# Kernel tuning notes

Hardware: AMD Instinct MI355X
Metric: run time of the kernel (lower is better)

Reference implementation:

```python
import jax, jax.numpy as jnp
from jax import lax
import numpy as np

EMBED_DIM = 512
KERNEL_SIZE = 8
B, S = 16, 4096


def setup_inputs() -> dict:
    key = jax.random.key(0)
    k1, k2, k3, k4, k5 = jax.random.split(key, 5)
    bound = 1.0 / np.sqrt(EMBED_DIM)
    x = jax.random.normal(k1, (B, S, EMBED_DIM), dtype=jnp.float32)
    W_ih = jax.random.uniform(k2, (EMBED_DIM, EMBED_DIM), jnp.float32, -bound, bound)
    W_hh = jax.random.uniform(k3, (EMBED_DIM, EMBED_DIM), jnp.float32, -bound, bound)
    b_ih = jax.random.uniform(k4, (EMBED_DIM,), jnp.float32, -bound, bound)
    b_hh = jax.random.uniform(k5, (EMBED_DIM,), jnp.float32, -bound, bound)
    return {"x": x, "W_ih": W_ih, "W_hh": W_hh, "b_ih": b_ih, "b_hh": b_hh}


def reference(x, W_ih, W_hh, b_ih, b_hh):
    # RNNPool.forward(x, mask=False): split seq into windows of KERNEL_SIZE,
    # run a vanilla tanh RNN (zero initial state) on each window, keep last h.
    Bd, Sd, E = x.shape
    stride = KERNEL_SIZE
    nw = Sd // stride
    # All windows are independent -> batch them: [B*nw, stride, E]
    xw = x.reshape(Bd * nw, stride, E)
    # Precompute input projection + both biases once: [B*nw, stride, E]
    pre = jnp.einsum("nte,he->nth", xw, W_ih) + (b_ih + b_hh)

    def step(h, p_t):
        h = jnp.tanh(p_t + h @ W_hh.T)
        return h, None

    h0 = jnp.zeros((Bd * nw, E), dtype=x.dtype)
    hT, _ = lax.scan(step, h0, jnp.swapaxes(pre, 0, 1))  # scan over stride steps
    return hT.reshape(Bd, nw, E)
```

## Files before the change

### kernel.cpp

```cpp
#include <hip/hip_runtime.h>
#include <hip/hip_bf16.h>
#include <stdint.h>


#define E_DIM 512
#define KSIZE 8
#define R_WIN 32
#define R_PRE 64
#define NBLK  256

typedef __attribute__((ext_vector_type(8))) _Float16       f16x8;
typedef __attribute__((ext_vector_type(4))) float          f32x4;
typedef __attribute__((ext_vector_type(4))) float          fv4;
typedef __attribute__((ext_vector_type(4))) unsigned short u16x4;
typedef __attribute__((ext_vector_type(8))) unsigned short u16x8;

typedef __attribute__((address_space(1))) const uint32_t glb_u32;
typedef __attribute__((address_space(3))) uint32_t       lds_u32;

__device__ __forceinline__ unsigned short f2h(float f) {
  return __builtin_bit_cast(unsigned short, (_Float16)f);
}
__device__ __forceinline__ float h2f(unsigned short u) {
  return (float)__builtin_bit_cast(_Float16, u);
}
__device__ __forceinline__ float tanh_fast(float v) {
  return 1.0f - 2.0f / (1.0f + __expf(2.0f * v));
}
__device__ __forceinline__ int swz(int row) { return (row ^ (row >> 1)) & 7; }

__global__ void pack_kernel(const float* __restrict__ Wih, const float* __restrict__ Whh,
                            const float* __restrict__ bih, const float* __restrict__ bhh,
                            unsigned short* __restrict__ wpack, float* __restrict__ bias) {
  int tid = blockIdx.x * 256 + threadIdx.x;
  int l = tid & 63;
  int s = (tid >> 6) & 15;
  int n = (tid >> 10) & 31;
  int m = tid >> 15;
  const float* W = m ? Whh : Wih;
  int row = n * 16 + (l & 15);
  int k0  = s * 32 + (l >> 4) * 8;
  const float* src = W + row * E_DIM + k0;
  u16x8 u;
  #pragma unroll
  for (int j = 0; j < 8; ++j) u[j] = f2h(src[j]);
  size_t dst = (((size_t)m * 16 + s) * 32 + n) * 512 + (size_t)l * 8;
  *reinterpret_cast<u16x8*>(wpack + dst) = u;
  if (tid < E_DIM) bias[tid] = bih[tid] + bhh[tid];
}

#define PRE_FRAG(bt, mt, nt) ((((size_t)(bt) * 2 + (mt)) * 32 + (nt)) * 256)

__global__ __launch_bounds__(512, 2)
void pre_kernel(const float* __restrict__ x,
                const unsigned short* __restrict__ wpack,
                const float* __restrict__ bias,
                unsigned short* __restrict__ prep) {
  __shared__ unsigned short x_lds[R_PRE * E_DIM];

  const int bt   = blockIdx.x;
  const int b    = bt >> 3;
  const int t    = bt & 7;
  const int w0   = b * R_PRE;
  const int tid  = threadIdx.x;
  const int lane = tid & 63;
  const int wid  = tid >> 6;
  const int l15  = lane & 15;
  const int a5   = lane >> 4;
  const int nt0  = wid * 4;

  float bias_r[4];
  #pragma unroll
  for (int n = 0; n < 4; ++n) bias_r[n] = bias[(nt0 + n) * 16 + l15];

  {
    const int srow = tid >> 3;
    const int sc   = tid & 7;
    const fv4* src4 = reinterpret_cast<const fv4*>(
        x + (size_t)((w0 + srow) * KSIZE + t) * E_DIM);
    #pragma unroll
    for (int j = 0; j < 16; ++j) {
      fv4 v = __builtin_nontemporal_load(&src4[sc + 8 * j]);
      int col  = (sc + 8 * j) * 4;
      int idx  = srow * E_DIM + (((col >> 3) ^ swz(srow)) << 3) + (col & 7);
      u16x4 u;
      u[0] = f2h(v.x); u[1] = f2h(v.y); u[2] = f2h(v.z); u[3] = f2h(v.w);
      *reinterpret_cast<u16x4*>(&x_lds[idx]) = u;
    }
  }
  __syncthreads();

  f32x4 acc[4][4];
  #pragma unroll
  for (int m = 0; m < 4; ++m)
    #pragma unroll
    for (int n = 0; n < 4; ++n) acc[m][n] = (f32x4){0.f, 0.f, 0.f, 0.f};

  #pragma unroll
  for (int s = 0; s < 16; ++s) {
    int u0 = s * 4 + a5;
    f16x8 A0, A1, A2, A3;
    {
      int r0 = l15,      i0 = r0 * E_DIM + ((u0 ^ swz(r0)) << 3);
      int r1 = 16 + l15, i1 = r1 * E_DIM + ((u0 ^ swz(r1)) << 3);
      int r2 = 32 + l15, i2 = r2 * E_DIM + ((u0 ^ swz(r2)) << 3);
      int r3 = 48 + l15, i3 = r3 * E_DIM + ((u0 ^ swz(r3)) << 3);
      A0 = *reinterpret_cast<const f16x8*>(&x_lds[i0]);
      A1 = *reinterpret_cast<const f16x8*>(&x_lds[i1]);
      A2 = *reinterpret_cast<const f16x8*>(&x_lds[i2]);
      A3 = *reinterpret_cast<const f16x8*>(&x_lds[i3]);
    }
    const unsigned short* wsl = wpack + ((size_t)s * 32 + nt0) * 512 + lane * 8;
    #pragma unroll
    for (int n = 0; n < 4; ++n) {
      f16x8 Bf = *reinterpret_cast<const f16x8*>(wsl + n * 512);
      acc[0][n] = __builtin_amdgcn_mfma_f32_16x16x32_f16(A0, Bf, acc[0][n], 0, 0, 0);
      acc[1][n] = __builtin_amdgcn_mfma_f32_16x16x32_f16(A1, Bf, acc[1][n], 0, 0, 0);
      acc[2][n] = __builtin_amdgcn_mfma_f32_16x16x32_f16(A2, Bf, acc[2][n], 0, 0, 0);
      acc[3][n] = __builtin_amdgcn_mfma_f32_16x16x32_f16(A3, Bf, acc[3][n], 0, 0, 0);
    }
  }

  #pragma unroll
  for (int m = 0; m < 4; ++m) {
    size_t bt_out = (size_t)(2 * b + (m >> 1)) * 8 + t;
    #pragma unroll
    for (int n = 0; n < 4; ++n) {
      u16x4 v;
      #pragma unroll
      for (int r = 0; r < 4; ++r) v[r] = f2h(acc[m][n][r] + bias_r[n]);
      __builtin_nontemporal_store(v,
          reinterpret_cast<u16x4*>(&prep[PRE_FRAG(bt_out, m & 1, nt0 + n) + lane * 4]));
    }
  }
}

__global__ __launch_bounds__(512, 2)
void rec_kernel(const unsigned short* __restrict__ prep,
                const unsigned short* __restrict__ wpack,
                float* __restrict__ out) {
  __shared__ unsigned short h_buf[2][R_WIN * E_DIM];
  __shared__ unsigned short w_ring[2][8 * 2048];

  const int b    = blockIdx.x;
  const int w0   = b * R_WIN;
  const int tid  = threadIdx.x;
  const int lane = tid & 63;
  const int wid  = tid >> 6;
  const int l15  = lane & 15;
  const int a5   = lane >> 4;
  const int nt0  = wid * 4;

  const char* wbase = (const char*)(wpack + ((size_t)16 * 32) * 512);
  #define STAGE(s, p)                                                               \
    do {                                                                            \
      const char* _src = wbase + (((size_t)(s) * 32 + nt0) * 1024) + lane * 16;     \
      unsigned short* _dst = &w_ring[p][wid * 2048];                                \
      __builtin_amdgcn_global_load_lds((glb_u32*)_src, (lds_u32*)_dst, 16, 0, 0);   \
      __builtin_amdgcn_global_load_lds((glb_u32*)(_src + 1024),                     \
                                       (lds_u32*)(_dst + 512), 16, 0, 0);           \
      __builtin_amdgcn_global_load_lds((glb_u32*)(_src + 2048),                     \
                                       (lds_u32*)(_dst + 1024), 16, 0, 0);          \
      __builtin_amdgcn_global_load_lds((glb_u32*)(_src + 3072),                     \
                                       (lds_u32*)(_dst + 1536), 16, 0, 0);          \
    } while (0)

  #pragma unroll
  for (int mt = 0; mt < 2; ++mt)
    #pragma unroll
    for (int n = 0; n < 4; ++n) {
      u16x4 p = __builtin_nontemporal_load(reinterpret_cast<const u16x4*>(
          &prep[PRE_FRAG(b * 8 + 0, mt, nt0 + n) + lane * 4]));
      int ncol = (nt0 + n) * 16 + l15;
      int ub = ncol >> 3, co = ncol & 7;
      #pragma unroll
      for (int r = 0; r < 4; ++r) {
        int row = mt * 16 + a5 * 4 + r;
        int idx = row * E_DIM + ((ub ^ swz(row)) << 3) + co;
        h_buf[0][idx] = f2h(tanh_fast(h2f(p[r])));
      }
    }

  u16x4 nxt[2][4];
  #pragma unroll
  for (int mt = 0; mt < 2; ++mt)
    #pragma unroll
    for (int n = 0; n < 4; ++n)
      nxt[mt][n] = __builtin_nontemporal_load(reinterpret_cast<const u16x4*>(
          &prep[PRE_FRAG(b * 8 + 1, mt, nt0 + n) + lane * 4]));

  __syncthreads();

  int cur = 0;
  for (int t = 1; t < KSIZE; ++t) {
    f32x4 acc[2][4];
    #pragma unroll
    for (int mt = 0; mt < 2; ++mt)
      #pragma unroll
      for (int n = 0; n < 4; ++n) {
        #pragma unroll
        for (int r = 0; r < 4; ++r) acc[mt][n][r] = h2f(nxt[mt][n][r]);
      }

    STAGE(0, 0);
    STAGE(1, 1);
    asm volatile("s_waitcnt vmcnt(4)" ::: "memory");
    f16x8 Wa0, Wa1, Wa2, Wa3, Ha0, Ha1;
    f16x8 Wb0, Wb1, Wb2, Wb3, Hb0, Hb1;
    {
      const unsigned short* wsl = &w_ring[0][wid * 2048 + lane * 8];
      Wa0 = *reinterpret_cast<const f16x8*>(wsl);
      Wa1 = *reinterpret_cast<const f16x8*>(wsl + 512);
      Wa2 = *reinterpret_cast<const f16x8*>(wsl + 1024);
      Wa3 = *reinterpret_cast<const f16x8*>(wsl + 1536);
      int ia0 = l15 * E_DIM + ((a5 ^ swz(l15)) << 3);
      int ia1 = (16 + l15) * E_DIM + ((a5 ^ swz(16 + l15)) << 3);
      Ha0 = *reinterpret_cast<const f16x8*>(&h_buf[cur][ia0]);
      Ha1 = *reinterpret_cast<const f16x8*>(&h_buf[cur][ia1]);
    }

    #pragma unroll
    for (int s = 0; s < 16; ++s) {
      asm volatile("s_waitcnt lgkmcnt(0)" ::: "memory");
      if (s + 2 < 16) STAGE(s + 2, (s + 2) & 1);
      if (s < 14)       asm volatile("s_waitcnt vmcnt(4)" ::: "memory");
      else if (s == 14) asm volatile("s_waitcnt vmcnt(0)" ::: "memory");
      if (s < 15) {
        const unsigned short* wsl = &w_ring[(s + 1) & 1][wid * 2048 + lane * 8];
        Wb0 = *reinterpret_cast<const f16x8*>(wsl);
        Wb1 = *reinterpret_cast<const f16x8*>(wsl + 512);
        Wb2 = *reinterpret_cast<const f16x8*>(wsl + 1024);
        Wb3 = *reinterpret_cast<const f16x8*>(wsl + 1536);
        int u0  = (s + 1) * 4 + a5;
        int ia0 = l15 * E_DIM + ((u0 ^ swz(l15)) << 3);
        int ia1 = (16 + l15) * E_DIM + ((u0 ^ swz(16 + l15)) << 3);
        Hb0 = *reinterpret_cast<const f16x8*>(&h_buf[cur][ia0]);
        Hb1 = *reinterpret_cast<const f16x8*>(&h_buf[cur][ia1]);
      }
      acc[0][0] = __builtin_amdgcn_mfma_f32_16x16x32_f16(Ha0, Wa0, acc[0][0], 0, 0, 0);
      acc[1][0] = __builtin_amdgcn_mfma_f32_16x16x32_f16(Ha1, Wa0, acc[1][0], 0, 0, 0);
      acc[0][1] = __builtin_amdgcn_mfma_f32_16x16x32_f16(Ha0, Wa1, acc[0][1], 0, 0, 0);
      acc[1][1] = __builtin_amdgcn_mfma_f32_16x16x32_f16(Ha1, Wa1, acc[1][1], 0, 0, 0);
      acc[0][2] = __builtin_amdgcn_mfma_f32_16x16x32_f16(Ha0, Wa2, acc[0][2], 0, 0, 0);
      acc[1][2] = __builtin_amdgcn_mfma_f32_16x16x32_f16(Ha1, Wa2, acc[1][2], 0, 0, 0);
      acc[0][3] = __builtin_amdgcn_mfma_f32_16x16x32_f16(Ha0, Wa3, acc[0][3], 0, 0, 0);
      acc[1][3] = __builtin_amdgcn_mfma_f32_16x16x32_f16(Ha1, Wa3, acc[1][3], 0, 0, 0);
      Wa0 = Wb0; Wa1 = Wb1; Wa2 = Wb2; Wa3 = Wb3;
      Ha0 = Hb0; Ha1 = Hb1;
    }

    if (t == KSIZE - 1) {
      #pragma unroll
      for (int mt = 0; mt < 2; ++mt)
        #pragma unroll
        for (int n = 0; n < 4; ++n) {
          int ncol = (nt0 + n) * 16 + l15;
          #pragma unroll
          for (int r = 0; r < 4; ++r) {
            int row = mt * 16 + a5 * 4 + r;
            out[(size_t)(w0 + row) * E_DIM + ncol] = tanh_fast(acc[mt][n][r]);
          }
        }
    } else {
      #pragma unroll
      for (int mt = 0; mt < 2; ++mt)
        #pragma unroll
        for (int n = 0; n < 4; ++n)
          nxt[mt][n] = __builtin_nontemporal_load(reinterpret_cast<const u16x4*>(
              &prep[PRE_FRAG(b * 8 + t + 1, mt, nt0 + n) + lane * 4]));

      int nb = cur ^ 1;
      #pragma unroll
      for (int mt = 0; mt < 2; ++mt)
        #pragma unroll
        for (int n = 0; n < 4; ++n) {
          int ncol = (nt0 + n) * 16 + l15;
          int ub = ncol >> 3, co = ncol & 7;
          #pragma unroll
          for (int r = 0; r < 4; ++r) {
            int row = mt * 16 + a5 * 4 + r;
            int idx = row * E_DIM + ((ub ^ swz(row)) << 3) + co;
            h_buf[nb][idx] = f2h(tanh_fast(acc[mt][n][r]));
          }
        }
      __syncthreads();
      cur = nb;
    }
  }
  #undef STAGE
}

__global__ __launch_bounds__(512, 1)
void rnnpool_fused(const float* __restrict__ x,
                   const unsigned short* __restrict__ wpack,
                   const float* __restrict__ bias,
                   float* __restrict__ out) {
  __shared__ unsigned short x_lds[R_WIN * E_DIM];
  __shared__ unsigned short h_lds[R_WIN * E_DIM];

  const int tid  = threadIdx.x;
  const int lane = tid & 63;
  const int wid  = tid >> 6;
  const int w0   = blockIdx.x * R_WIN;
  const int l15 = lane & 15;
  const int a5  = lane >> 4;
  const int nt0 = wid * 4;

  float bias_r[4];
  #pragma unroll
  for (int n = 0; n < 4; ++n) bias_r[n] = bias[(nt0 + n) * 16 + l15];

  const int srow = tid >> 4;
  const int sc4  = tid & 15;

  for (int t = 0; t < KSIZE; ++t) {
    {
      const fv4* src4 = reinterpret_cast<const fv4*>(
          x + (size_t)((w0 + srow) * KSIZE + t) * E_DIM);
      #pragma unroll
      for (int j = 0; j < 8; ++j) {
        fv4 v = src4[sc4 + 16 * j];
        int col  = (sc4 + 16 * j) * 4;
        int idx  = srow * E_DIM + (((col >> 3) ^ swz(srow)) << 3) + (col & 7);
        u16x4 u;
        u[0] = f2h(v.x); u[1] = f2h(v.y); u[2] = f2h(v.z); u[3] = f2h(v.w);
        *reinterpret_cast<u16x4*>(&x_lds[idx]) = u;
      }
    }
    __syncthreads();

    f32x4 acc[2][4];
    #pragma unroll
    for (int mt = 0; mt < 2; ++mt)
      #pragma unroll
      for (int n = 0; n < 4; ++n) acc[mt][n] = (f32x4){0.f, 0.f, 0.f, 0.f};

    #pragma unroll
    for (int s = 0; s < 16; ++s) {
      int u0 = s * 4 + a5;
      int ia = l15 * E_DIM + ((u0 ^ swz(l15)) << 3);
      f16x8 A0 = *reinterpret_cast<const f16x8*>(&x_lds[ia]);
      f16x8 A1 = *reinterpret_cast<const f16x8*>(&x_lds[ia + 16 * E_DIM]);
      const unsigned short* wsl = wpack + ((size_t)s * 32 + nt0) * 512 + lane * 8;
      #pragma unroll
      for (int n = 0; n < 4; ++n) {
        f16x8 Bf = *reinterpret_cast<const f16x8*>(wsl + n * 512);
        acc[0][n] = __builtin_amdgcn_mfma_f32_16x16x32_f16(A0, Bf, acc[0][n], 0, 0, 0);
        acc[1][n] = __builtin_amdgcn_mfma_f32_16x16x32_f16(A1, Bf, acc[1][n], 0, 0, 0);
      }
    }

    if (t > 0) {
      #pragma unroll
      for (int s = 0; s < 16; ++s) {
        int u0 = s * 4 + a5;
        int ia = l15 * E_DIM + ((u0 ^ swz(l15)) << 3);
        f16x8 H0 = *reinterpret_cast<const f16x8*>(&h_lds[ia]);
        f16x8 H1 = *reinterpret_cast<const f16x8*>(&h_lds[ia + 16 * E_DIM]);
        const unsigned short* wsl = wpack + ((size_t)(16 + s) * 32 + nt0) * 512 + lane * 8;
        #pragma unroll
        for (int n = 0; n < 4; ++n) {
          f16x8 Bf = *reinterpret_cast<const f16x8*>(wsl + n * 512);
          acc[0][n] = __builtin_amdgcn_mfma_f32_16x16x32_f16(H0, Bf, acc[0][n], 0, 0, 0);
          acc[1][n] = __builtin_amdgcn_mfma_f32_16x16x32_f16(H1, Bf, acc[1][n], 0, 0, 0);
        }
      }
    }
    __syncthreads();

    if (t == KSIZE - 1) {
      #pragma unroll
      for (int mt = 0; mt < 2; ++mt)
        #pragma unroll
        for (int n = 0; n < 4; ++n) {
          int ncol = (nt0 + n) * 16 + l15;
          #pragma unroll
          for (int r = 0; r < 4; ++r) {
            int row = mt * 16 + a5 * 4 + r;
            out[(size_t)(w0 + row) * E_DIM + ncol] = tanh_fast(acc[mt][n][r] + bias_r[n]);
          }
        }
    } else {
      #pragma unroll
      for (int mt = 0; mt < 2; ++mt)
        #pragma unroll
        for (int n = 0; n < 4; ++n) {
          int ncol = (nt0 + n) * 16 + l15;
          int ub = ncol >> 3, co = ncol & 7;
          #pragma unroll
          for (int r = 0; r < 4; ++r) {
            int row = mt * 16 + a5 * 4 + r;
            int idx = row * E_DIM + ((ub ^ swz(row)) << 3) + co;
            h_lds[idx] = f2h(tanh_fast(acc[mt][n][r] + bias_r[n]));
          }
        }
      __syncthreads();
    }
  }
}

extern "C" void kernel_launch(void* const* d_in, const int* in_sizes, int n_in,
                              void* d_out, int out_size, void* d_ws, size_t ws_size,
                              hipStream_t stream) {
  const float* x   = (const float*)d_in[0];
  const float* Wih = (const float*)d_in[1];
  const float* Whh = (const float*)d_in[2];
  const float* bih = (const float*)d_in[3];
  const float* bhh = (const float*)d_in[4];
  float* out = (float*)d_out;

  const size_t PRE_BYTES  = (size_t)33554432 * 2;
  const size_t WPK_BYTES  = (size_t)524288 * 2;
  const size_t NEED       = PRE_BYTES + WPK_BYTES + 4096;

  if (ws_size >= NEED) {
    unsigned short* prep  = (unsigned short*)d_ws;
    unsigned short* wpack = (unsigned short*)((char*)d_ws + PRE_BYTES);
    float*          bias  = (float*)((char*)d_ws + PRE_BYTES + WPK_BYTES);
    pack_kernel<<<256, 256, 0, stream>>>(Wih, Whh, bih, bhh, wpack, bias);
    pre_kernel<<<1024, 512, 0, stream>>>(x, wpack, bias, prep);
    rec_kernel<<<NBLK, 512, 0, stream>>>(prep, wpack, out);
  } else {
    unsigned short* wpack = (unsigned short*)d_ws;
    float*          bias  = (float*)((char*)d_ws + WPK_BYTES);
    pack_kernel<<<256, 256, 0, stream>>>(Wih, Whh, bih, bhh, wpack, bias);
    rnnpool_fused<<<NBLK, 512, 0, stream>>>(x, wpack, bias, out);
  }
}
```

Baseline: 152.8 us.

## Split recurrence blocks to 16 windows each and single-buffer hidden state

The recurrence kernel now handles 16 windows per block instead of 32, launching 512 blocks, and each wave does 4 MFMAs per k-step instead of 8. The hidden-state buffer in LDS drops from double to single buffering, with an extra barrier before it is overwritten, and launch bounds rise to allow 4 blocks per CU. The aim is more parallelism and occupancy across the 256 CUs. In exchange, every weight tile is streamed from L2 twice as often per window, and the extra barrier adds a sync per step.

```diff
diff --git a/kernel.cpp b/kernel.cpp
--- a/kernel.cpp
+++ b/kernel.cpp
@@ -5,9 +5,8 @@
 
 #define E_DIM 512
 #define KSIZE 8
-#define R_WIN 32
+#define R_REC 16
 #define R_PRE 64
-#define NBLK  256
 
 typedef __attribute__((ext_vector_type(8))) _Float16       f16x8;
 typedef __attribute__((ext_vector_type(4))) float          f32x4;
@@ -135,15 +134,17 @@
   }
 }
 
-__global__ __launch_bounds__(512, 2)
+__global__ __launch_bounds__(512, 4)
 void rec_kernel(const unsigned short* __restrict__ prep,
                 const unsigned short* __restrict__ wpack,
                 float* __restrict__ out) {
-  __shared__ unsigned short h_buf[2][R_WIN * E_DIM];
+  __shared__ unsigned short h_buf[R_REC * E_DIM];
   __shared__ unsigned short w_ring[2][8 * 2048];
 
-  const int b    = blockIdx.x;
-  const int w0   = b * R_WIN;
+  const int rb   = blockIdx.x;
+  const int gb   = rb >> 1;
+  const int mtb  = rb & 1;
+  const int w0   = rb * R_REC;
   const int tid  = threadIdx.x;
   const int lane = tid & 63;
   const int wid  = tid >> 6;
@@ -166,57 +167,48 @@
     } while (0)
 
   #pragma unroll
-  for (int mt = 0; mt < 2; ++mt)
+  for (int n = 0; n < 4; ++n) {
+    u16x4 p = __builtin_nontemporal_load(reinterpret_cast<const u16x4*>(
+        &prep[PRE_FRAG(gb * 8 + 0, mtb, nt0 + n) + lane * 4]));
+    int ncol = (nt0 + n) * 16 + l15;
+    int ub = ncol >> 3, co = ncol & 7;
+    #pragma unroll
+    for (int r = 0; r < 4; ++r) {
+      int row = a5 * 4 + r;
+      int idx = row * E_DIM + ((ub ^ swz(row)) << 3) + co;
+      h_buf[idx] = f2h(tanh_fast(h2f(p[r])));
+    }
+  }
+
+  u16x4 nxt[4];
+  #pragma unroll
+  for (int n = 0; n < 4; ++n)
+    nxt[n] = __builtin_nontemporal_load(reinterpret_cast<const u16x4*>(
+        &prep[PRE_FRAG(gb * 8 + 1, mtb, nt0 + n) + lane * 4]));
+
+  __syncthreads();
+
+  for (int t = 1; t < KSIZE; ++t) {
+    f32x4 acc[4];
     #pragma unroll
     for (int n = 0; n < 4; ++n) {
-      u16x4 p = __builtin_nontemporal_load(reinterpret_cast<const u16x4*>(
-          &prep[PRE_FRAG(b * 8 + 0, mt, nt0 + n) + lane * 4]));
-      int ncol = (nt0 + n) * 16 + l15;
-      int ub = ncol >> 3, co = ncol & 7;
-      #pragma unroll
-      for (int r = 0; r < 4; ++r) {
-        int row = mt * 16 + a5 * 4 + r;
-        int idx = row * E_DIM + ((ub ^ swz(row)) << 3) + co;
-        h_buf[0][idx] = f2h(tanh_fast(h2f(p[r])));
-      }
-    }
-
-  u16x4 nxt[2][4];
-  #pragma unroll
-  for (int mt = 0; mt < 2; ++mt)
-    #pragma unroll
-    for (int n = 0; n < 4; ++n)
-      nxt[mt][n] = __builtin_nontemporal_load(reinterpret_cast<const u16x4*>(
-          &prep[PRE_FRAG(b * 8 + 1, mt, nt0 + n) + lane * 4]));
-
-  __syncthreads();
-
-  int cur = 0;
-  for (int t = 1; t < KSIZE; ++t) {
-    f32x4 acc[2][4];
-    #pragma unroll
-    for (int mt = 0; mt < 2; ++mt)
-      #pragma unroll
-      for (int n = 0; n < 4; ++n) {
-        #pragma unroll
-        for (int r = 0; r < 4; ++r) acc[mt][n][r] = h2f(nxt[mt][n][r]);
-      }
+      #pragma unroll
+      for (int r = 0; r < 4; ++r) acc[n][r] = h2f(nxt[n][r]);
+    }
 
     STAGE(0, 0);
     STAGE(1, 1);
     asm volatile("s_waitcnt vmcnt(4)" ::: "memory");
-    f16x8 Wa0, Wa1, Wa2, Wa3, Ha0, Ha1;
-    f16x8 Wb0, Wb1, Wb2, Wb3, Hb0, Hb1;
+    f16x8 Wa0, Wa1, Wa2, Wa3, Ha;
+    f16x8 Wb0, Wb1, Wb2, Wb3, Hb;
     {
       const unsigned short* wsl = &w_ring[0][wid * 2048 + lane * 8];
       Wa0 = *reinterpret_cast<const f16x8*>(wsl);
       Wa1 = *reinterpret_cast<const f16x8*>(wsl + 512);
       Wa2 = *reinterpret_cast<const f16x8*>(wsl + 1024);
       Wa3 = *reinterpret_cast<const f16x8*>(wsl + 1536);
-      int ia0 = l15 * E_DIM + ((a5 ^ swz(l15)) << 3);
-      int ia1 = (16 + l15) * E_DIM + ((a5 ^ swz(16 + l15)) << 3);
-      Ha0 = *reinterpret_cast<const f16x8*>(&h_buf[cur][ia0]);
-      Ha1 = *reinterpret_cast<const f16x8*>(&h_buf[cur][ia1]);
+      int ia = l15 * E_DIM + ((a5 ^ swz(l15)) << 3);
+      Ha = *reinterpret_cast<const f16x8*>(&h_buf[ia]);
     }
 
     #pragma unroll
@@ -231,60 +223,48 @@
         Wb1 = *reinterpret_cast<const f16x8*>(wsl + 512);
         Wb2 = *reinterpret_cast<const f16x8*>(wsl + 1024);
         Wb3 = *reinterpret_cast<const f16x8*>(wsl + 1536);
-        int u0  = (s + 1) * 4 + a5;
-        int ia0 = l15 * E_DIM + ((u0 ^ swz(l15)) << 3);
-        int ia1 = (16 + l15) * E_DIM + ((u0 ^ swz(16 + l15)) << 3);
-        Hb0 = *reinterpret_cast<const f16x8*>(&h_buf[cur][ia0]);
-        Hb1 = *reinterpret_cast<const f16x8*>(&h_buf[cur][ia1]);
-      }
-      acc[0][0] = __builtin_amdgcn_mfma_f32_16x16x32_f16(Ha0, Wa0, acc[0][0], 0, 0, 0);
-      acc[1][0] = __builtin_amdgcn_mfma_f32_16x16x32_f16(Ha1, Wa0, acc[1][0], 0, 0, 0);
-      acc[0][1] = __builtin_amdgcn_mfma_f32_16x16x32_f16(Ha0, Wa1, acc[0][1], 0, 0, 0);
-      acc[1][1] = __builtin_amdgcn_mfma_f32_16x16x32_f16(Ha1, Wa1, acc[1][1], 0, 0, 0);
-      acc[0][2] = __builtin_amdgcn_mfma_f32_16x16x32_f16(Ha0, Wa2, acc[0][2], 0, 0, 0);
-      acc[1][2] = __builtin_amdgcn_mfma_f32_16x16x32_f16(Ha1, Wa2, acc[1][2], 0, 0, 0);
-      acc[0][3] = __builtin_amdgcn_mfma_f32_16x16x32_f16(Ha0, Wa3, acc[0][3], 0, 0, 0);
-      acc[1][3] = __builtin_amdgcn_mfma_f32_16x16x32_f16(Ha1, Wa3, acc[1][3], 0, 0, 0);
+        int u0 = (s + 1) * 4 + a5;
+        int ia = l15 * E_DIM + ((u0 ^ swz(l15)) << 3);
+        Hb = *reinterpret_cast<const f16x8*>(&h_buf[ia]);
+      }
+      acc[0] = __builtin_amdgcn_mfma_f32_16x16x32_f16(Ha, Wa0, acc[0], 0, 0, 0);
+      acc[1] = __builtin_amdgcn_mfma_f32_16x16x32_f16(Ha, Wa1, acc[1], 0, 0, 0);
+      acc[2] = __builtin_amdgcn_mfma_f32_16x16x32_f16(Ha, Wa2, acc[2], 0, 0, 0);
+      acc[3] = __builtin_amdgcn_mfma_f32_16x16x32_f16(Ha, Wa3, acc[3], 0, 0, 0);
       Wa0 = Wb0; Wa1 = Wb1; Wa2 = Wb2; Wa3 = Wb3;
-      Ha0 = Hb0; Ha1 = Hb1;
+      Ha = Hb;
     }
 
     if (t == KSIZE - 1) {
       #pragma unroll
-      for (int mt = 0; mt < 2; ++mt)
+      for (int n = 0; n < 4; ++n) {
+        int ncol = (nt0 + n) * 16 + l15;
         #pragma unroll
-        for (int n = 0; n < 4; ++n) {
-          int ncol = (nt0 + n) * 16 + l15;
-          #pragma unroll
-          for (int r = 0; r < 4; ++r) {
-            int row = mt * 16 + a5 * 4 + r;
-            out[(size_t)(w0 + row) * E_DIM + ncol] = tanh_fast(acc[mt][n][r]);
-          }
+        for (int r = 0; r < 4; ++r) {
+          int row = a5 * 4 + r;
+          out[(size_t)(w0 + row) * E_DIM + ncol] = tanh_fast(acc[n][r]);
         }
+      }
     } else {
-      #pragma unroll
-      for (int mt = 0; mt < 2; ++mt)
+      __syncthreads();
+
+      #pragma unroll
+      for (int n = 0; n < 4; ++n)
+        nxt[n] = __builtin_nontemporal_load(reinterpret_cast<const u16x4*>(
+            &prep[PRE_FRAG(gb * 8 + t + 1, mtb, nt0 + n) + lane * 4]));
+
+      #pragma unroll
+      for (int n = 0; n < 4; ++n) {
+        int ncol = (nt0 + n) * 16 + l15;
+        int ub = ncol >> 3, co = ncol & 7;
         #pragma unroll
-        for (int n = 0; n < 4; ++n)
-          nxt[mt][n] = __builtin_nontemporal_load(reinterpret_cast<const u16x4*>(
-              &prep[PRE_FRAG(b * 8 + t + 1, mt, nt0 + n) + lane * 4]));
-
-      int nb = cur ^ 1;
-      #pragma unroll
-      for (int mt = 0; mt < 2; ++mt)
-        #pragma unroll
-        for (int n = 0; n < 4; ++n) {
-          int ncol = (nt0 + n) * 16 + l15;
-          int ub = ncol >> 3, co = ncol & 7;
-          #pragma unroll
-          for (int r = 0; r < 4; ++r) {
-            int row = mt * 16 + a5 * 4 + r;
-            int idx = row * E_DIM + ((ub ^ swz(row)) << 3) + co;
-            h_buf[nb][idx] = f2h(tanh_fast(acc[mt][n][r]));
-          }
+        for (int r = 0; r < 4; ++r) {
+          int row = a5 * 4 + r;
+          int idx = row * E_DIM + ((ub ^ swz(row)) << 3) + co;
+          h_buf[idx] = f2h(tanh_fast(acc[n][r]));
         }
+      }
       __syncthreads();
-      cur = nb;
     }
   }
   #undef STAGE
@@ -295,13 +275,13 @@
                    const unsigned short* __restrict__ wpack,
                    const float* __restrict__ bias,
                    float* __restrict__ out) {
-  __shared__ unsigned short x_lds[R_WIN * E_DIM];
-  __shared__ unsigned short h_lds[R_WIN * E_DIM];
+  __shared__ unsigned short x_lds[32 * E_DIM];
+  __shared__ unsigned short h_lds[32 * E_DIM];
 
   const int tid  = threadIdx.x;
   const int lane = tid & 63;
   const int wid  = tid >> 6;
-  const int w0   = blockIdx.x * R_WIN;
+  const int w0   = blockIdx.x * 32;
   const int l15 = lane & 15;
   const int a5  = lane >> 4;
   const int nt0 = wid * 4;
@@ -419,11 +399,11 @@
     float*          bias  = (float*)((char*)d_ws + PRE_BYTES + WPK_BYTES);
     pack_kernel<<<256, 256, 0, stream>>>(Wih, Whh, bih, bhh, wpack, bias);
     pre_kernel<<<1024, 512, 0, stream>>>(x, wpack, bias, prep);
-    rec_kernel<<<NBLK, 512, 0, stream>>>(prep, wpack, out);
+    rec_kernel<<<512, 512, 0, stream>>>(prep, wpack, out);
   } else {
     unsigned short* wpack = (unsigned short*)d_ws;
     float*          bias  = (float*)((char*)d_ws + WPK_BYTES);
     pack_kernel<<<256, 256, 0, stream>>>(Wih, Whh, bih, bhh, wpack, bias);
-    rnnpool_fused<<<NBLK, 512, 0, stream>>>(x, wpack, bias, out);
-  }
-}
+    rnnpool_fused<<<256, 512, 0, stream>>>(x, wpack, bias, out);
+  }
+}
```

Measured after the change: 270.0 us. 76.7% more time.
